# Performance work log

Measured on AMD Instinct MI355X. Metric: run time of the kernel, lower is better.

## Reference

```python
import jax, jax.numpy as jnp
import numpy as np

N = 12288      # num_nodes
D = 128        # seg_emb
NUM_GRAPHS = 48
NUM_CLS = 27   # classes 24,25,26 are excluded by the module


def setup_inputs() -> dict:
    key = jax.random.key(0)
    k1, k2, k3, k4 = jax.random.split(key, 4)
    z1 = jax.random.normal(k1, (N, D), dtype=jnp.float32)
    z2 = jax.random.normal(k2, (N, D), dtype=jnp.float32)
    cls_label = jax.random.randint(k3, (N,), 0, NUM_CLS, dtype=jnp.int32)
    batch = jnp.sort(jax.random.randint(k4, (N,), 0, NUM_GRAPHS, dtype=jnp.int32))
    return {"z1": z1, "z2": z2, "cls_label": cls_label, "batch": batch}


def reference(z1, z2, cls_label, batch):
    # Pairwise validity mask: same graph AND same class AND class not in {24,25,26}.
    # This reproduces the nested gather->matmul->scatter loops: each (graph, class)
    # block of z1 @ z2.T is kept, everything else stays zero. Single-node classes
    # (skipped in the original) only contribute a diagonal entry, which is zeroed.
    same_graph = batch[:, None] == batch[None, :]            # [N, N]
    same_cls = cls_label[:, None] == cls_label[None, :]      # [N, N]
    excluded = (cls_label >= 24) & (cls_label <= 26)         # [N]
    mask = same_graph & same_cls & ~excluded[:, None]

    scores = jnp.matmul(z1, z2.T)                            # [N, N] inner products
    out = jnp.where(mask, scores, jnp.float32(0.0))
    n = out.shape[0]
    idx = jnp.arange(n)
    out = out.at[idx, idx].set(0.0)                          # zero the diagonal
    return out
```

## Files before the change

kernel.cpp:

```cpp
#include <hip/hip_runtime.h>

#define NN 12288
#define DD 128
#define NG 48

typedef float v4f __attribute__((ext_vector_type(4)));

__global__ __launch_bounds__(256) void build_starts(
    const int* __restrict__ batch, int* __restrict__ start)
{
    for (int j = threadIdx.x; j <= NN; j += 256) {
        if (j == NN) {
            const int b = batch[NN - 1];
            for (int g = b + 1; g <= NG; ++g) start[g] = NN;
        } else {
            const int b = batch[j];
            const int bprev = (j == 0) ? -1 : batch[j - 1];
            for (int g = bprev + 1; g <= b; ++g) start[g] = j;
        }
    }
}

__global__ __launch_bounds__(256) void segdec_main(
    const float* __restrict__ z1, const float* __restrict__ z2,
    const int* __restrict__ cls, const int* __restrict__ batch,
    const int* __restrict__ start, float* __restrict__ out)
{
    const int bid = (int)blockIdx.x;
    const int tid = (int)threadIdx.x;
    const v4f zero4 = {0.f, 0.f, 0.f, 0.f};

    if (bid % 5 == 0) {
        const int z = bid / 5;
        #pragma unroll
        for (int r = 0; r < 4; ++r) {
            const int i = (z << 2) + r;
            const int b = batch[i];
            const int lo = start[b];
            const int hi = start[b + 1];
            const int c0 = lo >> 2;
            const int c1 = (hi - 1) >> 2;
            v4f* __restrict__ orow = reinterpret_cast<v4f*>(out + (size_t)i * NN);
            #pragma unroll
            for (int k = 0; k < 12; ++k) {
                const int c = tid + (k << 8);
                if (c < c0 || c > c1) orow[c] = zero4;
            }
        }
    } else {
        const int i = bid - bid / 5 - 1;
        const int cls_i = cls[i];
        const int b = batch[i];
        const int lo = start[b];
        const int hi = start[b + 1];
        const int c0 = lo >> 2;
        const int c1 = (hi - 1) >> 2;
        const int jbase = c0 << 2;
        const int ncols = ((c1 + 1) << 2) - jbase;

        const v4f* __restrict__ za = reinterpret_cast<const v4f*>(z1 + (size_t)i * DD);
        float* __restrict__ orow = out + (size_t)i * NN;

        for (int t = tid; t < ncols; t += 256) {
            const int j = jbase + t;
            float s = 0.f;
            if (cls_i < 24 && j >= lo && j < hi && j != i && cls[j] == cls_i) {
                const v4f* __restrict__ zb =
                    reinterpret_cast<const v4f*>(z2 + (size_t)j * DD);
                #pragma unroll
                for (int d = 0; d < DD / 4; ++d) {
                    const v4f a = za[d];
                    const v4f b4 = zb[d];
                    s = fmaf(a.x, b4.x, s);
                    s = fmaf(a.y, b4.y, s);
                    s = fmaf(a.z, b4.z, s);
                    s = fmaf(a.w, b4.w, s);
                }
            }
            orow[j] = s;
        }
    }
}

extern "C" void kernel_launch(void* const* d_in, const int* in_sizes, int n_in,
                              void* d_out, int out_size, void* d_ws, size_t ws_size,
                              hipStream_t stream) {
    const float* z1    = (const float*)d_in[0];
    const float* z2    = (const float*)d_in[1];
    const int*   cls   = (const int*)d_in[2];
    const int*   batch = (const int*)d_in[3];
    float*       out   = (float*)d_out;
    int*         start = (int*)d_ws;

    build_starts<<<1, 256, 0, stream>>>(batch, start);
    segdec_main<<<NN + NN / 4, 256, 0, stream>>>(z1, z2, cls, batch, start, out);
}
```

Before: 648.9 us.

## Zero output with memset and scatter only valid same-class dot products

```diff
diff --git a/kernel.cpp b/kernel.cpp
--- a/kernel.cpp
+++ b/kernel.cpp
@@ -21,61 +21,35 @@
     }
 }
 
-__global__ __launch_bounds__(256) void segdec_main(
+__global__ __launch_bounds__(64) void band_fill(
     const float* __restrict__ z1, const float* __restrict__ z2,
     const int* __restrict__ cls, const int* __restrict__ batch,
     const int* __restrict__ start, float* __restrict__ out)
 {
-    const int bid = (int)blockIdx.x;
-    const int tid = (int)threadIdx.x;
-    const v4f zero4 = {0.f, 0.f, 0.f, 0.f};
+    const int i = (int)blockIdx.x;
+    const int cls_i = cls[i];
+    if (cls_i >= 24) return;
 
-    if (bid % 5 == 0) {
-        const int z = bid / 5;
-        #pragma unroll
-        for (int r = 0; r < 4; ++r) {
-            const int i = (z << 2) + r;
-            const int b = batch[i];
-            const int lo = start[b];
-            const int hi = start[b + 1];
-            const int c0 = lo >> 2;
-            const int c1 = (hi - 1) >> 2;
-            v4f* __restrict__ orow = reinterpret_cast<v4f*>(out + (size_t)i * NN);
+    const int b  = batch[i];
+    const int lo = start[b];
+    const int hi = start[b + 1];
+
+    const v4f* __restrict__ za = reinterpret_cast<const v4f*>(z1 + (size_t)i * DD);
+    float* __restrict__ orow = out + (size_t)i * NN;
+
+    for (int j = lo + (int)threadIdx.x; j < hi; j += 64) {
+        if (j != i && cls[j] == cls_i) {
+            const v4f* __restrict__ zb =
+                reinterpret_cast<const v4f*>(z2 + (size_t)j * DD);
+            float s = 0.f;
             #pragma unroll
-            for (int k = 0; k < 12; ++k) {
-                const int c = tid + (k << 8);
-                if (c < c0 || c > c1) orow[c] = zero4;
-            }
-        }
-    } else {
-        const int i = bid - bid / 5 - 1;
-        const int cls_i = cls[i];
-        const int b = batch[i];
-        const int lo = start[b];
-        const int hi = start[b + 1];
-        const int c0 = lo >> 2;
-        const int c1 = (hi - 1) >> 2;
-        const int jbase = c0 << 2;
-        const int ncols = ((c1 + 1) << 2) - jbase;
-
-        const v4f* __restrict__ za = reinterpret_cast<const v4f*>(z1 + (size_t)i * DD);
-        float* __restrict__ orow = out + (size_t)i * NN;
-
-        for (int t = tid; t < ncols; t += 256) {
-            const int j = jbase + t;
-            float s = 0.f;
-            if (cls_i < 24 && j >= lo && j < hi && j != i && cls[j] == cls_i) {
-                const v4f* __restrict__ zb =
-                    reinterpret_cast<const v4f*>(z2 + (size_t)j * DD);
-                #pragma unroll
-                for (int d = 0; d < DD / 4; ++d) {
-                    const v4f a = za[d];
-                    const v4f b4 = zb[d];
-                    s = fmaf(a.x, b4.x, s);
-                    s = fmaf(a.y, b4.y, s);
-                    s = fmaf(a.z, b4.z, s);
-                    s = fmaf(a.w, b4.w, s);
-                }
+            for (int d = 0; d < DD / 4; ++d) {
+                const v4f a  = za[d];
+                const v4f b4 = zb[d];
+                s = fmaf(a.x, b4.x, s);
+                s = fmaf(a.y, b4.y, s);
+                s = fmaf(a.z, b4.z, s);
+                s = fmaf(a.w, b4.w, s);
             }
             orow[j] = s;
         }
@@ -92,6 +66,7 @@
     float*       out   = (float*)d_out;
     int*         start = (int*)d_ws;
 
+    hipMemsetAsync(out, 0, (size_t)NN * NN * sizeof(float), stream);
     build_starts<<<1, 256, 0, stream>>>(batch, start);
-    segdec_main<<<NN + NN / 4, 256, 0, stream>>>(z1, z2, cls, batch, start, out);
+    band_fill<<<NN, 64, 0, stream>>>(z1, z2, cls, batch, start, out);
 }
```

Measured after the change: 656.0 us. No clear change (+1.1%).
